# Performance work log

Measured on AMD Instinct MI355X. Metric: run time of the kernel, lower is better.

Reference implementation:

```python
import jax, jax.numpy as jnp
import numpy as np

SEQ, BATCH, IN_DIM, HID = 512, 64, 512, 1024


def setup_inputs() -> dict:
    key = jax.random.key(0)
    k1, k2, k3, k4, k5 = jax.random.split(key, 5)
    s = 1.0 / np.sqrt(HID)
    return {
        "embedding": jax.random.normal(k1, (SEQ, BATCH, IN_DIM), dtype=jnp.float32),
        "w_ih": jax.random.normal(k2, (3 * HID, IN_DIM), dtype=jnp.float32) * s,
        "w_hh": jax.random.normal(k3, (3 * HID, HID), dtype=jnp.float32) * s,
        "b_ih": jax.random.normal(k4, (3 * HID,), dtype=jnp.float32) * s,
        "b_hh": jax.random.normal(k5, (3 * HID,), dtype=jnp.float32) * s,
    }


def _gru_scan(embedding, w_ih, w_hh, b_ih, b_hh):
    # Precompute input projections for all timesteps in one GEMM: (S, B, 3H)
    gi_all = jnp.einsum('sbi,gi->sbg', embedding, w_ih) + b_ih
    hid = w_hh.shape[1]

    def step(h, gi):
        gh = h @ w_hh.T + b_hh                      # (B, 3H)
        i_r, i_z, i_n = jnp.split(gi, 3, axis=-1)
        h_r, h_z, h_n = jnp.split(gh, 3, axis=-1)
        r = jax.nn.sigmoid(i_r + h_r)
        z = jax.nn.sigmoid(i_z + h_z)
        n = jnp.tanh(i_n + r * h_n)
        h_new = (1.0 - z) * n + z * h
        return h_new, h_new

    h0 = jnp.zeros((embedding.shape[1], hid), dtype=embedding.dtype)
    h_last, hs = jax.lax.scan(step, h0, gi_all)     # hs: (S, B, H)
    return hs, h_last


def reference(embedding, w_ih, w_hh, b_ih, b_hh):
    hs, h_last = _gru_scan(embedding, w_ih, w_hh, b_ih, b_hh)
    outputs = jnp.transpose(hs, (1, 0, 2))          # (B, S, H) like permute(1,0,2)
    hidden = h_last[None, :, :]                     # (1, B, H) like nn.GRU hidden
    return outputs, hidden
```

## Files before the change

kernel.cpp:

```cpp
#include <hip/hip_runtime.h>
#include <hip/hip_bf16.h>

#define SEQ 512
#define BATCH 64
#define IN_DIM 512
#define HID 1024
#define G3 3072
#define MTOT 32768
#define GB 16
#define UPW 32

typedef float f32x4 __attribute__((ext_vector_type(4)));
typedef short s16x8 __attribute__((ext_vector_type(8)));

static __device__ __forceinline__ unsigned short f2bf(float f) {
  union { float f; unsigned u; } v; v.f = f;
  unsigned r = v.u + 0x7fffu + ((v.u >> 16) & 1u);
  return (unsigned short)(r >> 16);
}
static __device__ __forceinline__ float bf2f(unsigned short b) {
  union { unsigned u; float f; } v; v.u = ((unsigned)b) << 16;
  return v.f;
}
static __device__ __forceinline__ unsigned umin2(unsigned a, unsigned b) { return a < b ? a : b; }

__global__ __launch_bounds__(256) void split_kernel(const float* __restrict__ src,
    unsigned short* __restrict__ hi, unsigned short* __restrict__ lo, int n4) {
  int stride = gridDim.x * blockDim.x;
  for (int i = blockIdx.x * blockDim.x + threadIdx.x; i < n4; i += stride) {
    float4 v = ((const float4*)src)[i];
    ushort4 h, l;
    h.x = f2bf(v.x); l.x = f2bf(v.x - bf2f(h.x));
    h.y = f2bf(v.y); l.y = f2bf(v.y - bf2f(h.y));
    h.z = f2bf(v.z); l.z = f2bf(v.z - bf2f(h.z));
    h.w = f2bf(v.w); l.w = f2bf(v.w - bf2f(h.w));
    ((ushort4*)hi)[i] = h;
    ((ushort4*)lo)[i] = l;
  }
}


#define LDH(dst, OFFS) asm volatile("global_load_dwordx4 %0, %1, off offset:" OFFS " sc0 sc1" : "=v"(dst) : "v"(hadr))
#define WAITV(N) do { asm volatile("s_waitcnt vmcnt(" #N ")" ::: "memory"); __builtin_amdgcn_sched_barrier(0); } while (0)

__global__ __launch_bounds__(512, 2) void gru_fused(
    const unsigned short* __restrict__ Whh_hi,
    const unsigned short* __restrict__ emb_hi, const unsigned short* __restrict__ emb_lo,
    const unsigned short* __restrict__ wih_hi, const unsigned short* __restrict__ wih_lo,
    const float* __restrict__ bih,
    float* __restrict__ gi32, unsigned short* __restrict__ gi16, int gi_is_f32,
    const float* __restrict__ bhh,
    unsigned short* __restrict__ h0, unsigned short* __restrict__ h1,
    unsigned* __restrict__ bar,
    float* __restrict__ out, float* __restrict__ hidden)
{
  __shared__ float ghp[8][16][100];
  __shared__ unsigned short Ah[128 * 64];
  __shared__ unsigned short Alo_[128 * 64];
  __shared__ unsigned short Bh[128 * 64];
  __shared__ unsigned short Blo_[128 * 64];
  const int tid = threadIdx.x;
  const int wg = blockIdx.x;
  const int wave = tid >> 6, lane = tid & 63;
  const int row16 = lane & 15;

  unsigned* cnt = bar;
  unsigned* cA = bar + 256;
  unsigned* genv = bar + 768;

  if (wg >= 128) {
    const int widx = wg - 128;
    const int wm = (wave >> 2) * 64, wn = (wave & 3) * 32;
    const int kq = lane >> 4;
    const int srow = tid >> 3;
    const int skc = tid & 7;

    for (int it = 0; it < 48; ++it) {
      int q = widx + it * 128;
      int bm = q / 24, bn = q - bm * 24;
      int bm0 = bm * 128, bn0 = bn * 128;

      f32x4 acc[4][2] = {};
      for (int kt = 0; kt < IN_DIM / 64; ++kt) {
        uint4 rah[2], ral[2], rbh[2], rbl[2];
        for (int i = 0; i < 2; ++i) {
          int r = i * 64 + srow;
          size_t ao = (size_t)(bm0 + r) * IN_DIM + kt * 64 + skc * 8;
          size_t bo = (size_t)(bn0 + r) * IN_DIM + kt * 64 + skc * 8;
          rah[i] = *(const uint4*)&emb_hi[ao];
          ral[i] = *(const uint4*)&emb_lo[ao];
          rbh[i] = *(const uint4*)&wih_hi[bo];
          rbl[i] = *(const uint4*)&wih_lo[bo];
        }
        __syncthreads();
        for (int i = 0; i < 2; ++i) {
          int r = i * 64 + srow;
          *(uint4*)&Ah[r * 64 + skc * 8]   = rah[i];
          *(uint4*)&Alo_[r * 64 + skc * 8] = ral[i];
          *(uint4*)&Bh[r * 64 + skc * 8]   = rbh[i];
          *(uint4*)&Blo_[r * 64 + skc * 8] = rbl[i];
        }
        __syncthreads();
        for (int kk = 0; kk < 2; ++kk) {
          s16x8 ah[4], al[4], bh[2], bl[2];
          for (int mi = 0; mi < 4; ++mi) {
            int off = (wm + mi * 16 + row16) * 64 + kk * 32 + kq * 8;
            ah[mi] = *(const s16x8*)&Ah[off];
            al[mi] = *(const s16x8*)&Alo_[off];
          }
          for (int ni = 0; ni < 2; ++ni) {
            int off = (wn + ni * 16 + row16) * 64 + kk * 32 + kq * 8;
            bh[ni] = *(const s16x8*)&Bh[off];
            bl[ni] = *(const s16x8*)&Blo_[off];
          }
          for (int mi = 0; mi < 4; ++mi)
            for (int ni = 0; ni < 2; ++ni) {
              acc[mi][ni] = __builtin_amdgcn_mfma_f32_16x16x32_bf16(ah[mi], bh[ni], acc[mi][ni], 0, 0, 0);
              acc[mi][ni] = __builtin_amdgcn_mfma_f32_16x16x32_bf16(al[mi], bh[ni], acc[mi][ni], 0, 0, 0);
              acc[mi][ni] = __builtin_amdgcn_mfma_f32_16x16x32_bf16(ah[mi], bl[ni], acc[mi][ni], 0, 0, 0);
            }
        }
      }
      for (int mi = 0; mi < 4; ++mi) {
        int grow0 = bm0 + wm + mi * 16 + kq * 4;
        for (int ni = 0; ni < 2; ++ni) {
          int gcol = bn0 + wn + ni * 16 + row16;
          float bias = bih[gcol];
#pragma unroll
          for (int qq = 0; qq < 4; ++qq) {
            float v = acc[mi][ni][qq] + bias;
            size_t off = (size_t)(grow0 + qq) * G3 + gcol;
            if (gi_is_f32) {
              unsigned long long ad = (unsigned long long)(gi32 + off);
              asm volatile("global_store_dword %0, %1, off sc0 sc1" :: "v"(ad), "v"(v) : "memory");
            } else {
              unsigned short bv = f2bf(v);
              unsigned long long ad = (unsigned long long)(gi16 + off);
              asm volatile("global_store_short %0, %1, off sc0 sc1" :: "v"(ad), "v"(bv) : "memory");
            }
          }
        }
      }
      asm volatile("s_waitcnt vmcnt(0)" ::: "memory");
      __syncthreads();
      if (tid == 0)
        __hip_atomic_fetch_add(&cnt[bm], 1u, __ATOMIC_RELAXED, __HIP_MEMORY_SCOPE_AGENT);
    }
    return;
  }

  const int g = wg >> 5, w = wg & 31;
  const int j0 = w * UPW;
  const int b0 = g * GB;
  const int kw = wave;
  const int koc = lane >> 4;

  s16x8 wr[24];
#pragma unroll
  for (int t = 0; t < 6; ++t) {
#pragma unroll
    for (int ck = 0; ck < 4; ++ck) {
      int wrow = (t >> 1) * HID + j0 + (t & 1) * 16 + row16;
      size_t byte = (size_t)wrow * 2048 + (size_t)(kw * 256 + ck * 64 + koc * 16);
      wr[t * 4 + ck] = *(const s16x8*)((const char*)Whh_hi + byte);
    }
  }

  const unsigned hvoff = (unsigned)((b0 + row16) * 2048 + kw * 256 + koc * 16);
  const int bb_l = tid >> 5, uu_l = tid & 31;
  const int bb = b0 + bb_l, j = j0 + uu_l;
  const float bh_r = bhh[j], bh_z = bhh[HID + j], bh_n = bhh[2 * HID + j];
  float hprev = 0.f;
  const int sub = w >> 4;

  for (int s = 0; s < SEQ; ++s) {
    const unsigned short* hin = (s & 1) ? h1 : h0;
    unsigned short* hout = (s & 1) ? h0 : h1;
    unsigned long long hadr = (unsigned long long)hin + hvoff;

    if (tid == 0) {
      unsigned long long gva = (unsigned long long)(genv + g * 32);
      unsigned long long cva = (unsigned long long)(cnt + (s >> 1));
      for (;;) {
        uint2 gg; unsigned cc;
        asm volatile("global_load_dwordx2 %0, %2, off sc0 sc1\n\t"
                     "global_load_dword %1, %3, off sc0 sc1\n\t"
                     "s_waitcnt vmcnt(0)"
                     : "=v"(gg), "=v"(cc) : "v"(gva), "v"(cva) : "memory");
        if (umin2(gg.x, gg.y) >= (unsigned)s && cc >= 24u) break;
      }
    }
    __syncthreads();

    float gir = 0.f, giz = 0.f, gin_ = 0.f;
    unsigned short g16r = 0, g16z = 0, g16n = 0;
    if (gi_is_f32) {
      unsigned long long ga = (unsigned long long)(gi32 + (size_t)(s * BATCH + bb) * G3 + j);
      asm volatile("global_load_dword %0, %1, off sc0 sc1" : "=v"(gir) : "v"(ga));
      asm volatile("global_load_dword %0, %1, off sc0 sc1" : "=v"(giz) : "v"(ga + 4096ull));
      asm volatile("global_load_dword %0, %1, off sc0 sc1" : "=v"(gin_) : "v"(ga + 8192ull));
    } else {
      unsigned long long ga = (unsigned long long)(gi16 + (size_t)(s * BATCH + bb) * G3 + j);
      asm volatile("global_load_ushort %0, %1, off sc0 sc1" : "=v"(g16r) : "v"(ga));
      asm volatile("global_load_ushort %0, %1, off sc0 sc1" : "=v"(g16z) : "v"(ga + 2048ull));
      asm volatile("global_load_ushort %0, %1, off sc0 sc1" : "=v"(g16n) : "v"(ga + 4096ull));
    }

    f32x4 acc[6] = {};
    s16x8 a0, a1, a2, a3;
    LDH(a0, "0"); LDH(a1, "64"); LDH(a2, "128"); LDH(a3, "192");
    WAITV(3);
#pragma unroll
    for (int t = 0; t < 6; ++t) acc[t] = __builtin_amdgcn_mfma_f32_16x16x32_bf16(a0, wr[t * 4 + 0], acc[t], 0, 0, 0);
    WAITV(2);
#pragma unroll
    for (int t = 0; t < 6; ++t) acc[t] = __builtin_amdgcn_mfma_f32_16x16x32_bf16(a1, wr[t * 4 + 1], acc[t], 0, 0, 0);
    WAITV(1);
#pragma unroll
    for (int t = 0; t < 6; ++t) acc[t] = __builtin_amdgcn_mfma_f32_16x16x32_bf16(a2, wr[t * 4 + 2], acc[t], 0, 0, 0);
    WAITV(0);
#pragma unroll
    for (int t = 0; t < 6; ++t) acc[t] = __builtin_amdgcn_mfma_f32_16x16x32_bf16(a3, wr[t * 4 + 3], acc[t], 0, 0, 0);

#pragma unroll
    for (int t = 0; t < 6; ++t)
#pragma unroll
      for (int qq = 0; qq < 4; ++qq)
        ghp[kw][koc * 4 + qq][t * 16 + row16] = acc[t][qq];
    __syncthreads();

    float ghr = 0.f, ghz = 0.f, ghn = 0.f;
#pragma unroll
    for (int k2 = 0; k2 < 8; ++k2) {
      ghr += ghp[k2][bb_l][uu_l];
      ghz += ghp[k2][bb_l][32 + uu_l];
      ghn += ghp[k2][bb_l][64 + uu_l];
    }
    float ir, iz, inn;
    if (gi_is_f32) { ir = gir; iz = giz; inn = gin_; }
    else { ir = bf2f(g16r); iz = bf2f(g16z); inn = bf2f(g16n); }
    float r = 1.f / (1.f + __expf(-(ir + ghr + bh_r)));
    float z = 1.f / (1.f + __expf(-(iz + ghz + bh_z)));
    float n = tanhf(inn + r * (ghn + bh_n));
    float h = (1.f - z) * n + z * hprev;
    hprev = h;
    unsigned short hb = f2bf(h);
    unsigned long long sha = (unsigned long long)hout + (unsigned)(bb * 1024 + j) * 2u;
    asm volatile("global_store_short %0, %1, off sc0 sc1" :: "v"(sha), "v"(hb) : "memory");
    out[((size_t)bb * SEQ + s) * HID + j] = h;
    if (s == SEQ - 1) hidden[(size_t)bb * HID + j] = h;
    asm volatile("s_waitcnt vmcnt(1)" ::: "memory");
    __syncthreads();

    if (tid == 0) {
      unsigned a = __hip_atomic_fetch_add(&cA[(g * 2 + sub) * 32], 1u, __ATOMIC_RELAXED, __HIP_MEMORY_SCOPE_AGENT);
      if (a + 1u == 16u * (unsigned)(s + 1)) {
        __hip_atomic_store(&genv[g * 32 + sub], (unsigned)(s + 1), __ATOMIC_RELAXED, __HIP_MEMORY_SCOPE_AGENT);
      }
    }
  }
}

extern "C" void kernel_launch(void* const* d_in, const int* in_sizes, int n_in,
                              void* d_out, int out_size, void* d_ws, size_t ws_size,
                              hipStream_t stream) {
  const float* emb = (const float*)d_in[0];
  const float* wih = (const float*)d_in[1];
  const float* whh = (const float*)d_in[2];
  const float* bih = (const float*)d_in[3];
  const float* bhh = (const float*)d_in[4];
  float* out = (float*)d_out;
  float* hidden = out + (size_t)BATCH * SEQ * HID;

  char* ws = (char*)d_ws;
  size_t off = 0;
  auto alloc = [&](size_t bytes) {
    char* p = ws + off;
    off += (bytes + 255) & ~(size_t)255;
    return p;
  };

  unsigned short* emb_hi = (unsigned short*)alloc((size_t)MTOT * IN_DIM * 2);
  unsigned short* emb_lo = (unsigned short*)alloc((size_t)MTOT * IN_DIM * 2);
  unsigned short* wih_hi = (unsigned short*)alloc((size_t)G3 * IN_DIM * 2);
  unsigned short* wih_lo = (unsigned short*)alloc((size_t)G3 * IN_DIM * 2);
  unsigned short* whh_hi = (unsigned short*)alloc((size_t)G3 * HID * 2);
  unsigned short* whh_lo = (unsigned short*)alloc((size_t)G3 * HID * 2);
  unsigned short* hbuf   = (unsigned short*)alloc((size_t)2 * BATCH * HID * 2);
  unsigned* bar = (unsigned*)alloc(8192);

  size_t gi32_bytes = (size_t)MTOT * G3 * 4;
  int gi_is_f32 = (off + gi32_bytes <= ws_size) ? 1 : 0;
  float* gi32 = nullptr;
  unsigned short* gi16 = nullptr;
  if (gi_is_f32) gi32 = (float*)alloc(gi32_bytes);
  else           gi16 = (unsigned short*)alloc((size_t)MTOT * G3 * 2);

  split_kernel<<<4096, 256, 0, stream>>>(emb, emb_hi, emb_lo, MTOT * IN_DIM / 4);
  split_kernel<<<1536, 256, 0, stream>>>(wih, wih_hi, wih_lo, G3 * IN_DIM / 4);
  split_kernel<<<3072, 256, 0, stream>>>(whh, whh_hi, whh_lo, G3 * HID / 4);

  (void)hipMemsetAsync(hbuf, 0, (size_t)2 * BATCH * HID * 2, stream);
  (void)hipMemsetAsync(bar, 0, 8192, stream);

  size_t BH = (size_t)BATCH * HID;
  unsigned short* h0 = hbuf;
  unsigned short* h1 = hbuf + BH;
  void* args[] = { &whh_hi, &emb_hi, &emb_lo, &wih_hi, &wih_lo, &bih,
                   &gi32, &gi16, &gi_is_f32, &bhh,
                   &h0, &h1, &bar, &out, &hidden };
  (void)hipLaunchCooperativeKernel((void*)gru_fused, dim3(256), dim3(512), args, 0, stream);
}
```

Before: 2.082 ms.

## Split each batch group into two half-groups with staggered barriers

Each workgroup now runs every timestep as two sub-steps over 8-row halves of its 16-batch group. Each half has its own generation counter and cross-workgroup barrier, so the second half's matvec can overlap with other workgroups finishing the first half. The aim is to shorten the critical-path barrier wait. In exchange, every step issues twice the MFMAs (each wasting half of the 16 rows), adds a second barrier per step, and leaves half the threads idle in the gate phase.

```diff
diff --git a/kernel.cpp b/kernel.cpp
--- a/kernel.cpp
+++ b/kernel.cpp
@@ -54,7 +54,7 @@
     unsigned* __restrict__ bar,
     float* __restrict__ out, float* __restrict__ hidden)
 {
-  __shared__ float ghp[8][16][100];
+  __shared__ float ghp[8][8][100];
   __shared__ unsigned short Ah[128 * 64];
   __shared__ unsigned short Alo_[128 * 64];
   __shared__ unsigned short Bh[128 * 64];
@@ -151,7 +151,6 @@
 
   const int g = wg >> 5, w = wg & 31;
   const int j0 = w * UPW;
-  const int b0 = g * GB;
   const int kw = wave;
   const int koc = lane >> 4;
 
@@ -166,96 +165,191 @@
     }
   }
 
-  const unsigned hvoff = (unsigned)((b0 + row16) * 2048 + kw * 256 + koc * 16);
+  const int bA = g * GB, bB = g * GB + 8;
+  const unsigned hvA = (unsigned)((bA + (row16 & 7)) * 2048 + kw * 256 + koc * 16);
+  const unsigned hvB = (unsigned)((bB + (row16 & 7)) * 2048 + kw * 256 + koc * 16);
   const int bb_l = tid >> 5, uu_l = tid & 31;
-  const int bb = b0 + bb_l, j = j0 + uu_l;
-  const float bh_r = bhh[j], bh_z = bhh[HID + j], bh_n = bhh[2 * HID + j];
-  float hprev = 0.f;
-  const int sub = w >> 4;
+  const bool gat = (tid < 256);
+  const int jg = j0 + uu_l;
+  float bh_r = 0.f, bh_z = 0.f, bh_n = 0.f;
+  if (gat) { bh_r = bhh[jg]; bh_z = bhh[HID + jg]; bh_n = bhh[2 * HID + jg]; }
+  float hprevA = 0.f, hprevB = 0.f;
+  const int half = w >> 4;
 
   for (int s = 0; s < SEQ; ++s) {
     const unsigned short* hin = (s & 1) ? h1 : h0;
     unsigned short* hout = (s & 1) ? h0 : h1;
-    unsigned long long hadr = (unsigned long long)hin + hvoff;
 
     if (tid == 0) {
-      unsigned long long gva = (unsigned long long)(genv + g * 32);
-      unsigned long long cva = (unsigned long long)(cnt + (s >> 1));
+      if ((s & 1) == 0) {
+        unsigned long long cva = (unsigned long long)(cnt + (s >> 1));
+        for (;;) {
+          unsigned cc;
+          asm volatile("global_load_dword %0, %1, off sc0 sc1\n\ts_waitcnt vmcnt(0)"
+                       : "=v"(cc) : "v"(cva) : "memory");
+          if (cc >= 24u) break;
+        }
+      }
+      unsigned long long gva = (unsigned long long)(genv + (g * 2 + 0) * 32);
       for (;;) {
-        uint2 gg; unsigned cc;
-        asm volatile("global_load_dwordx2 %0, %2, off sc0 sc1\n\t"
-                     "global_load_dword %1, %3, off sc0 sc1\n\t"
-                     "s_waitcnt vmcnt(0)"
-                     : "=v"(gg), "=v"(cc) : "v"(gva), "v"(cva) : "memory");
-        if (umin2(gg.x, gg.y) >= (unsigned)s && cc >= 24u) break;
+        uint2 gg;
+        asm volatile("global_load_dwordx2 %0, %1, off sc0 sc1\n\ts_waitcnt vmcnt(0)"
+                     : "=v"(gg) : "v"(gva) : "memory");
+        if (umin2(gg.x, gg.y) >= (unsigned)s) break;
       }
     }
     __syncthreads();
 
-    float gir = 0.f, giz = 0.f, gin_ = 0.f;
-    unsigned short g16r = 0, g16z = 0, g16n = 0;
-    if (gi_is_f32) {
-      unsigned long long ga = (unsigned long long)(gi32 + (size_t)(s * BATCH + bb) * G3 + j);
-      asm volatile("global_load_dword %0, %1, off sc0 sc1" : "=v"(gir) : "v"(ga));
-      asm volatile("global_load_dword %0, %1, off sc0 sc1" : "=v"(giz) : "v"(ga + 4096ull));
-      asm volatile("global_load_dword %0, %1, off sc0 sc1" : "=v"(gin_) : "v"(ga + 8192ull));
-    } else {
-      unsigned long long ga = (unsigned long long)(gi16 + (size_t)(s * BATCH + bb) * G3 + j);
-      asm volatile("global_load_ushort %0, %1, off sc0 sc1" : "=v"(g16r) : "v"(ga));
-      asm volatile("global_load_ushort %0, %1, off sc0 sc1" : "=v"(g16z) : "v"(ga + 2048ull));
-      asm volatile("global_load_ushort %0, %1, off sc0 sc1" : "=v"(g16n) : "v"(ga + 4096ull));
-    }
-
-    f32x4 acc[6] = {};
-    s16x8 a0, a1, a2, a3;
-    LDH(a0, "0"); LDH(a1, "64"); LDH(a2, "128"); LDH(a3, "192");
-    WAITV(3);
-#pragma unroll
-    for (int t = 0; t < 6; ++t) acc[t] = __builtin_amdgcn_mfma_f32_16x16x32_bf16(a0, wr[t * 4 + 0], acc[t], 0, 0, 0);
-    WAITV(2);
-#pragma unroll
-    for (int t = 0; t < 6; ++t) acc[t] = __builtin_amdgcn_mfma_f32_16x16x32_bf16(a1, wr[t * 4 + 1], acc[t], 0, 0, 0);
-    WAITV(1);
-#pragma unroll
-    for (int t = 0; t < 6; ++t) acc[t] = __builtin_amdgcn_mfma_f32_16x16x32_bf16(a2, wr[t * 4 + 2], acc[t], 0, 0, 0);
-    WAITV(0);
-#pragma unroll
-    for (int t = 0; t < 6; ++t) acc[t] = __builtin_amdgcn_mfma_f32_16x16x32_bf16(a3, wr[t * 4 + 3], acc[t], 0, 0, 0);
-
-#pragma unroll
-    for (int t = 0; t < 6; ++t)
-#pragma unroll
-      for (int qq = 0; qq < 4; ++qq)
-        ghp[kw][koc * 4 + qq][t * 16 + row16] = acc[t][qq];
+    float girA = 0.f, gizA = 0.f, ginA = 0.f, girB = 0.f, gizB = 0.f, ginB = 0.f;
+    unsigned short r16A = 0, z16A = 0, n16A = 0, r16B = 0, z16B = 0, n16B = 0;
+    if (gat) {
+      if (gi_is_f32) {
+        unsigned long long gaA = (unsigned long long)(gi32 + (size_t)(s * BATCH + bA + bb_l) * G3 + jg);
+        unsigned long long gaB = (unsigned long long)(gi32 + (size_t)(s * BATCH + bB + bb_l) * G3 + jg);
+        asm volatile("global_load_dword %0, %1, off sc0 sc1" : "=v"(girA) : "v"(gaA));
+        asm volatile("global_load_dword %0, %1, off sc0 sc1" : "=v"(gizA) : "v"(gaA + 4096ull));
+        asm volatile("global_load_dword %0, %1, off sc0 sc1" : "=v"(ginA) : "v"(gaA + 8192ull));
+        asm volatile("global_load_dword %0, %1, off sc0 sc1" : "=v"(girB) : "v"(gaB));
+        asm volatile("global_load_dword %0, %1, off sc0 sc1" : "=v"(gizB) : "v"(gaB + 4096ull));
+        asm volatile("global_load_dword %0, %1, off sc0 sc1" : "=v"(ginB) : "v"(gaB + 8192ull));
+      } else {
+        unsigned long long gaA = (unsigned long long)(gi16 + (size_t)(s * BATCH + bA + bb_l) * G3 + jg);
+        unsigned long long gaB = (unsigned long long)(gi16 + (size_t)(s * BATCH + bB + bb_l) * G3 + jg);
+        asm volatile("global_load_ushort %0, %1, off sc0 sc1" : "=v"(r16A) : "v"(gaA));
+        asm volatile("global_load_ushort %0, %1, off sc0 sc1" : "=v"(z16A) : "v"(gaA + 2048ull));
+        asm volatile("global_load_ushort %0, %1, off sc0 sc1" : "=v"(n16A) : "v"(gaA + 4096ull));
+        asm volatile("global_load_ushort %0, %1, off sc0 sc1" : "=v"(r16B) : "v"(gaB));
+        asm volatile("global_load_ushort %0, %1, off sc0 sc1" : "=v"(z16B) : "v"(gaB + 2048ull));
+        asm volatile("global_load_ushort %0, %1, off sc0 sc1" : "=v"(n16B) : "v"(gaB + 4096ull));
+      }
+    }
+
+    {
+      unsigned long long hadr = (unsigned long long)hin + hvA;
+      f32x4 acc[6] = {};
+      s16x8 a0, a1, a2, a3;
+      LDH(a0, "0"); LDH(a1, "64"); LDH(a2, "128"); LDH(a3, "192");
+      WAITV(3);
+#pragma unroll
+      for (int t = 0; t < 6; ++t) acc[t] = __builtin_amdgcn_mfma_f32_16x16x32_bf16(a0, wr[t * 4 + 0], acc[t], 0, 0, 0);
+      WAITV(2);
+#pragma unroll
+      for (int t = 0; t < 6; ++t) acc[t] = __builtin_amdgcn_mfma_f32_16x16x32_bf16(a1, wr[t * 4 + 1], acc[t], 0, 0, 0);
+      WAITV(1);
+#pragma unroll
+      for (int t = 0; t < 6; ++t) acc[t] = __builtin_amdgcn_mfma_f32_16x16x32_bf16(a2, wr[t * 4 + 2], acc[t], 0, 0, 0);
+      WAITV(0);
+#pragma unroll
+      for (int t = 0; t < 6; ++t) acc[t] = __builtin_amdgcn_mfma_f32_16x16x32_bf16(a3, wr[t * 4 + 3], acc[t], 0, 0, 0);
+
+      if (koc < 2) {
+#pragma unroll
+        for (int t = 0; t < 6; ++t)
+#pragma unroll
+          for (int qq = 0; qq < 4; ++qq)
+            ghp[kw][koc * 4 + qq][t * 16 + row16] = acc[t][qq];
+      }
+      __syncthreads();
+
+      if (gat) {
+        float ghr = 0.f, ghz = 0.f, ghn = 0.f;
+#pragma unroll
+        for (int k2 = 0; k2 < 8; ++k2) {
+          ghr += ghp[k2][bb_l][uu_l];
+          ghz += ghp[k2][bb_l][32 + uu_l];
+          ghn += ghp[k2][bb_l][64 + uu_l];
+        }
+        float ir, iz, inn;
+        if (gi_is_f32) { ir = girA; iz = gizA; inn = ginA; }
+        else { ir = bf2f(r16A); iz = bf2f(z16A); inn = bf2f(n16A); }
+        float r = 1.f / (1.f + __expf(-(ir + ghr + bh_r)));
+        float z = 1.f / (1.f + __expf(-(iz + ghz + bh_z)));
+        float n = tanhf(inn + r * (ghn + bh_n));
+        float h = (1.f - z) * n + z * hprevA;
+        hprevA = h;
+        int bb = bA + bb_l;
+        unsigned short hb = f2bf(h);
+        unsigned long long sha = (unsigned long long)hout + (unsigned)(bb * 1024 + jg) * 2u;
+        asm volatile("global_store_short %0, %1, off sc0 sc1" :: "v"(sha), "v"(hb) : "memory");
+        out[((size_t)bb * SEQ + s) * HID + jg] = h;
+        if (s == SEQ - 1) hidden[(size_t)bb * HID + jg] = h;
+      }
+      asm volatile("s_waitcnt vmcnt(1)" ::: "memory");
+      __syncthreads();
+      if (tid == 0) {
+        unsigned a = __hip_atomic_fetch_add(&cA[(g * 4 + half) * 32], 1u, __ATOMIC_RELAXED, __HIP_MEMORY_SCOPE_AGENT);
+        if (a + 1u == 16u * (unsigned)(s + 1))
+          __hip_atomic_store(&genv[(g * 2 + 0) * 32 + half], (unsigned)(s + 1), __ATOMIC_RELAXED, __HIP_MEMORY_SCOPE_AGENT);
+      }
+    }
+
+    if (tid == 0) {
+      unsigned long long gva = (unsigned long long)(genv + (g * 2 + 1) * 32);
+      for (;;) {
+        uint2 gg;
+        asm volatile("global_load_dwordx2 %0, %1, off sc0 sc1\n\ts_waitcnt vmcnt(0)"
+                     : "=v"(gg) : "v"(gva) : "memory");
+        if (umin2(gg.x, gg.y) >= (unsigned)s) break;
+      }
+    }
     __syncthreads();
 
-    float ghr = 0.f, ghz = 0.f, ghn = 0.f;
-#pragma unroll
-    for (int k2 = 0; k2 < 8; ++k2) {
-      ghr += ghp[k2][bb_l][uu_l];
-      ghz += ghp[k2][bb_l][32 + uu_l];
-      ghn += ghp[k2][bb_l][64 + uu_l];
-    }
-    float ir, iz, inn;
-    if (gi_is_f32) { ir = gir; iz = giz; inn = gin_; }
-    else { ir = bf2f(g16r); iz = bf2f(g16z); inn = bf2f(g16n); }
-    float r = 1.f / (1.f + __expf(-(ir + ghr + bh_r)));
-    float z = 1.f / (1.f + __expf(-(iz + ghz + bh_z)));
-    float n = tanhf(inn + r * (ghn + bh_n));
-    float h = (1.f - z) * n + z * hprev;
-    hprev = h;
-    unsigned short hb = f2bf(h);
-    unsigned long long sha = (unsigned long long)hout + (unsigned)(bb * 1024 + j) * 2u;
-    asm volatile("global_store_short %0, %1, off sc0 sc1" :: "v"(sha), "v"(hb) : "memory");
-    out[((size_t)bb * SEQ + s) * HID + j] = h;
-    if (s == SEQ - 1) hidden[(size_t)bb * HID + j] = h;
-    asm volatile("s_waitcnt vmcnt(1)" ::: "memory");
-    __syncthreads();
-
-    if (tid == 0) {
-      unsigned a = __hip_atomic_fetch_add(&cA[(g * 2 + sub) * 32], 1u, __ATOMIC_RELAXED, __HIP_MEMORY_SCOPE_AGENT);
-      if (a + 1u == 16u * (unsigned)(s + 1)) {
-        __hip_atomic_store(&genv[g * 32 + sub], (unsigned)(s + 1), __ATOMIC_RELAXED, __HIP_MEMORY_SCOPE_AGENT);
+    {
+      unsigned long long hadr = (unsigned long long)hin + hvB;
+      f32x4 acc[6] = {};
+      s16x8 a0, a1, a2, a3;
+      LDH(a0, "0"); LDH(a1, "64"); LDH(a2, "128"); LDH(a3, "192");
+      WAITV(3);
+#pragma unroll
+      for (int t = 0; t < 6; ++t) acc[t] = __builtin_amdgcn_mfma_f32_16x16x32_bf16(a0, wr[t * 4 + 0], acc[t], 0, 0, 0);
+      WAITV(2);
+#pragma unroll
+      for (int t = 0; t < 6; ++t) acc[t] = __builtin_amdgcn_mfma_f32_16x16x32_bf16(a1, wr[t * 4 + 1], acc[t], 0, 0, 0);
+      WAITV(1);
+#pragma unroll
+      for (int t = 0; t < 6; ++t) acc[t] = __builtin_amdgcn_mfma_f32_16x16x32_bf16(a2, wr[t * 4 + 2], acc[t], 0, 0, 0);
+      WAITV(0);
+#pragma unroll
+      for (int t = 0; t < 6; ++t) acc[t] = __builtin_amdgcn_mfma_f32_16x16x32_bf16(a3, wr[t * 4 + 3], acc[t], 0, 0, 0);
+
+      if (koc < 2) {
+#pragma unroll
+        for (int t = 0; t < 6; ++t)
+#pragma unroll
+          for (int qq = 0; qq < 4; ++qq)
+            ghp[kw][koc * 4 + qq][t * 16 + row16] = acc[t][qq];
+      }
+      __syncthreads();
+
+      if (gat) {
+        float ghr = 0.f, ghz = 0.f, ghn = 0.f;
+#pragma unroll
+        for (int k2 = 0; k2 < 8; ++k2) {
+          ghr += ghp[k2][bb_l][uu_l];
+          ghz += ghp[k2][bb_l][32 + uu_l];
+          ghn += ghp[k2][bb_l][64 + uu_l];
+        }
+        float ir, iz, inn;
+        if (gi_is_f32) { ir = girB; iz = gizB; inn = ginB; }
+        else { ir = bf2f(r16B); iz = bf2f(z16B); inn = bf2f(n16B); }
+        float r = 1.f / (1.f + __expf(-(ir + ghr + bh_r)));
+        float z = 1.f / (1.f + __expf(-(iz + ghz + bh_z)));
+        float n = tanhf(inn + r * (ghn + bh_n));
+        float h = (1.f - z) * n + z * hprevB;
+        hprevB = h;
+        int bb = bB + bb_l;
+        unsigned short hb = f2bf(h);
+        unsigned long long sha = (unsigned long long)hout + (unsigned)(bb * 1024 + jg) * 2u;
+        asm volatile("global_store_short %0, %1, off sc0 sc1" :: "v"(sha), "v"(hb) : "memory");
+        out[((size_t)bb * SEQ + s) * HID + jg] = h;
+        if (s == SEQ - 1) hidden[(size_t)bb * HID + jg] = h;
+      }
+      asm volatile("s_waitcnt vmcnt(1)" ::: "memory");
+      __syncthreads();
+      if (tid == 0) {
+        unsigned a = __hip_atomic_fetch_add(&cA[(g * 4 + 2 + half) * 32], 1u, __ATOMIC_RELAXED, __HIP_MEMORY_SCOPE_AGENT);
+        if (a + 1u == 16u * (unsigned)(s + 1))
+          __hip_atomic_store(&genv[(g * 2 + 1) * 32 + half], (unsigned)(s + 1), __ATOMIC_RELAXED, __HIP_MEMORY_SCOPE_AGENT);
       }
     }
   }
```

After: 3.196 ms. 53.5% more time.
